# Kernel tuning notes

Measured on AMD Instinct MI355X. Metric: run time of the kernel, lower is better.

## Reference

```python
import jax, jax.numpy as jnp
import numpy as np

I_SIZE = 2048
O_SIZE = 2048
NUM_DOMAINS = 20
B, T = 16, 2048


def setup_inputs() -> dict:
    key = jax.random.key(0)
    k_x, k_w, k_d = jax.random.split(key, 3)
    x = jax.random.normal(k_x, (B, T, I_SIZE), dtype=jnp.float32)
    domain_id = jax.random.randint(k_d, (B,), 0, NUM_DOMAINS)
    # xavier_uniform over [num_domains, O*I]
    limit = float(np.sqrt(6.0 / (NUM_DOMAINS + O_SIZE * I_SIZE)))
    fc_weight = jax.random.uniform(k_w, (NUM_DOMAINS, O_SIZE * I_SIZE), dtype=jnp.float32, minval=-limit, maxval=limit)
    bias_weight = jnp.zeros((NUM_DOMAINS, O_SIZE), dtype=jnp.float32)
    return {"x": x, "domain_id": domain_id, "fc_weight": fc_weight, "bias_weight": bias_weight}


def reference(x, domain_id, fc_weight, bias_weight):
    # Gather per-sample weights: [B, I, O] (flat row reshaped as (I, O))
    W = fc_weight[domain_id].reshape(-1, I_SIZE, O_SIZE)
    b = bias_weight[domain_id]  # [B, O]
    # y = x @ W + b : [B, T, O]
    y = jnp.einsum('bti,bio->bto', x, W) + b[:, None, :]
    return y
```

## Files before the change

### kernel.cpp

```cpp
#include <hip/hip_runtime.h>
#include <hip/hip_bf16.h>
#include <stdint.h>

typedef __attribute__((ext_vector_type(4))) float  f32x4;
typedef __attribute__((ext_vector_type(8))) short  s16x8;
typedef __attribute__((ext_vector_type(4))) short  s16x4;

constexpr int I_SZ = 2048;
constexpr int O_SZ = 2048;
constexpr int T_SZ = 2048;
constexpr int B_MAX = 16;

constexpr size_t XT_ELEMS = (size_t)B_MAX * T_SZ * I_SZ;
constexpr size_t WT_ELEMS = (size_t)B_MAX * I_SZ * O_SZ;
constexpr size_t WS_NEEDED = (XT_ELEMS + WT_ELEMS) * sizeof(short);

__device__ __forceinline__ short f2bf(float f) {
    __hip_bfloat16 h = __float2bfloat16(f);
    return *reinterpret_cast<short*>(&h);
}

__device__ __forceinline__ void gload_lds16(const void* g, void* l) {
    __builtin_amdgcn_global_load_lds(
        (const __attribute__((address_space(1))) unsigned int*)g,
        (__attribute__((address_space(3))) unsigned int*)l, 16, 0, 0);
}

__global__ __launch_bounds__(256) void convA(const float* __restrict__ x,
                                             short* __restrict__ xt) {
    const int c = blockIdx.x * 256 + threadIdx.x;
    const int l  = c & 63;
    const int mi = (c >> 6) & 7;
    const int kt = (c >> 9) & 63;
    const int rest = c >> 15;
    const int mt = rest & 15, bz = rest >> 4;
    const int lr = l & 15, hi = l >> 4;
    const int m = mt * 128 + mi * 16 + lr;
    const float* src = x + ((size_t)(bz * T_SZ + m)) * I_SZ + kt * 32 + 4 * hi;
    f32x4 a = *reinterpret_cast<const f32x4*>(src);
    f32x4 b = *reinterpret_cast<const f32x4*>(src + 16);
    s16x8 h = { f2bf(a[0]), f2bf(a[1]), f2bf(a[2]), f2bf(a[3]),
                f2bf(b[0]), f2bf(b[1]), f2bf(b[2]), f2bf(b[3]) };
    *reinterpret_cast<s16x8*>(xt + (size_t)c * 8) = h;
}

__global__ __launch_bounds__(256) void convB(const float* __restrict__ fcw,
                                             const int* __restrict__ dom_id,
                                             short* __restrict__ wt) {
    const int c = blockIdx.x * 256 + threadIdx.x;
    const int l  = c & 63;
    const int ni = (c >> 6) & 7;
    const int kt = (c >> 9) & 63;
    const int rest = c >> 15;
    const int nt = rest & 15, bz = rest >> 4;
    const int lr = l & 15, hi = l >> 4;
    const int n = nt * 128 + ni * 16 + lr;
    const int dom = dom_id[bz];
    const float* src = fcw + (size_t)dom * ((size_t)I_SZ * O_SZ)
                           + (size_t)(kt * 32 + 4 * hi) * O_SZ + n;
    short h[8];
    #pragma unroll
    for (int j = 0; j < 4; ++j) {
        h[j]     = f2bf(src[(size_t)j * O_SZ]);
        h[4 + j] = f2bf(src[(size_t)(16 + j) * O_SZ]);
    }
    *reinterpret_cast<s16x8*>(wt + (size_t)c * 8) =
        *reinterpret_cast<s16x8*>(h);
}

__global__ __launch_bounds__(256, 2) void gemm_128x256(
        const short* __restrict__ xt, const short* __restrict__ wt,
        const float* __restrict__ bw, const int* __restrict__ dom_id,
        float* __restrict__ out) {
    __shared__ short As[2][8192];

    const int bid = blockIdx.x;
    const int swz = (bid & 7) * 256 + (bid >> 3);
    const int bz = swz >> 7;
    const int mb = (swz >> 3) & 15;
    const int nb = swz & 7;

    const int t = threadIdx.x;
    const int wv = t >> 6, l = t & 63;
    const int lr = l & 15, hi = l >> 4;
    const int nti  = wv >> 1;
    const int bsub = (wv & 1) * 4;

    const short* Abase = xt + (size_t)(bz * 16 + mb) * 64 * 4096;
    const short* Bp = wt + (size_t)((bz * 16 + nb * 2 + nti) * 64) * 4096
                         + bsub * 512 + l * 8;

    auto stageA = [&](int buf, int T) {
        #pragma unroll
        for (int r = 0; r < 4; ++r)
            gload_lds16(Abase + (size_t)(2 * T) * 4096 + r * 2048 + t * 8,
                        &As[buf][r * 2048 + t * 8]);
    };

    f32x4 acc[8][4] = {};

    stageA(0, 0);
    asm volatile("s_waitcnt vmcnt(0)" ::: "memory");
    asm volatile("s_barrier" ::: "memory");

    for (int T = 0; T < 32; ++T) {
        const int d = T & 1;

        s16x8 bq0[4], bq1[4];
        {
            const short* b0 = Bp + (size_t)(2 * T) * 4096;
            #pragma unroll
            for (int g = 0; g < 4; ++g)
                bq0[g] = *reinterpret_cast<const s16x8*>(b0 + g * 512);
            #pragma unroll
            for (int g = 0; g < 4; ++g)
                bq1[g] = *reinterpret_cast<const s16x8*>(b0 + 4096 + g * 512);
        }

        if (T + 1 < 32) stageA(d ^ 1, T + 1);

        s16x8 af[8];
        #pragma unroll
        for (int f = 0; f < 8; ++f)
            af[f] = *reinterpret_cast<const s16x8*>(&As[d][f * 512 + l * 8]);
        __builtin_amdgcn_s_setprio(1);
        #pragma unroll
        for (int f = 0; f < 8; ++f)
            #pragma unroll
            for (int g = 0; g < 4; ++g)
                acc[f][g] = __builtin_amdgcn_mfma_f32_16x16x32_bf16(
                                af[f], bq0[g], acc[f][g], 0, 0, 0);
        __builtin_amdgcn_s_setprio(0);

        #pragma unroll
        for (int f = 0; f < 8; ++f)
            af[f] = *reinterpret_cast<const s16x8*>(&As[d][4096 + f * 512 + l * 8]);
        __builtin_amdgcn_s_setprio(1);
        #pragma unroll
        for (int f = 0; f < 8; ++f)
            #pragma unroll
            for (int g = 0; g < 4; ++g)
                acc[f][g] = __builtin_amdgcn_mfma_f32_16x16x32_bf16(
                                af[f], bq1[g], acc[f][g], 0, 0, 0);
        __builtin_amdgcn_s_setprio(0);

        asm volatile("s_waitcnt vmcnt(0)" ::: "memory");
        asm volatile("s_barrier" ::: "memory");
    }

    const int dom = dom_id[bz];
    const int col0 = nb * 256 + wv * 64;
    float bias[4];
    #pragma unroll
    for (int g = 0; g < 4; ++g)
        bias[g] = bw[dom * O_SZ + col0 + g * 16 + lr];

    const size_t obase = ((size_t)bz * T_SZ + mb * 128) * O_SZ + col0;
    #pragma unroll
    for (int f = 0; f < 8; ++f) {
        #pragma unroll
        for (int r = 0; r < 4; ++r) {
            const int row = f * 16 + hi * 4 + r;
            float* orow = out + obase + (size_t)row * O_SZ;
            #pragma unroll
            for (int g = 0; g < 4; ++g)
                orow[g * 16 + lr] = acc[f][g][r] + bias[g];
        }
    }
}

constexpr int BM = 128, BN = 128, BK = 32;
constexpr int LDK = 40;
constexpr int NKT = I_SZ / BK;

__global__ __launch_bounds__(256) void dal_gemm(
    const float* __restrict__ x, const int* __restrict__ dom_id,
    const float* __restrict__ fcw, const float* __restrict__ bw,
    float* __restrict__ out)
{
    __shared__ short As[2][BM * LDK];
    __shared__ short Bs[2][BN * LDK];
    const int bz = blockIdx.z;
    const int m0 = blockIdx.y * BM, n0 = blockIdx.x * BN;
    const int dom = dom_id[bz];
    const float* Ag = x + ((size_t)bz * T_SZ + m0) * I_SZ;
    const float* Wg = fcw + (size_t)dom * ((size_t)I_SZ * O_SZ) + n0;
    const int t = threadIdx.x;
    const int am = t >> 3, ac = (t & 7) << 2;
    const int bk = (t >> 5) << 2, bn = (t & 31) << 2;
    const int wv = t >> 6, lane = t & 63;
    const int wr = (wv >> 1) << 6, wc = (wv & 1) << 6;
    const int hi = lane >> 4, lr = lane & 15;
    f32x4 acc[4][4] = {};
    f32x4 ra[4], rb[4];
    auto load_tile = [&](int kb) {
        #pragma unroll
        for (int p = 0; p < 4; ++p)
            ra[p] = *reinterpret_cast<const f32x4*>(Ag + (size_t)(am + 32 * p) * I_SZ + kb + ac);
        #pragma unroll
        for (int r = 0; r < 4; ++r)
            rb[r] = *reinterpret_cast<const f32x4*>(Wg + (size_t)(kb + bk + r) * O_SZ + bn);
    };
    auto store_tile = [&](int buf) {
        #pragma unroll
        for (int p = 0; p < 4; ++p) {
            s16x4 h = { f2bf(ra[p][0]), f2bf(ra[p][1]), f2bf(ra[p][2]), f2bf(ra[p][3]) };
            *reinterpret_cast<s16x4*>(&As[buf][(am + 32 * p) * LDK + ac]) = h;
        }
        #pragma unroll
        for (int i = 0; i < 4; ++i) {
            s16x4 h = { f2bf(rb[0][i]), f2bf(rb[1][i]), f2bf(rb[2][i]), f2bf(rb[3][i]) };
            *reinterpret_cast<s16x4*>(&Bs[buf][(bn + i) * LDK + bk]) = h;
        }
    };
    load_tile(0);
    store_tile(0);
    __syncthreads();
    for (int kt = 0; kt < NKT; ++kt) {
        const int cur = kt & 1;
        if (kt + 1 < NKT) load_tile((kt + 1) * BK);
        s16x8 af[4], bfr[4];
        #pragma unroll
        for (int im = 0; im < 4; ++im) {
            const short* p = &As[cur][(wr + im * 16 + lr) * LDK + 4 * hi];
            s16x4 lo = *reinterpret_cast<const s16x4*>(p);
            s16x4 hh = *reinterpret_cast<const s16x4*>(p + 16);
            af[im] = __builtin_shufflevector(lo, hh, 0, 1, 2, 3, 4, 5, 6, 7);
        }
        #pragma unroll
        for (int in = 0; in < 4; ++in) {
            const short* p = &Bs[cur][(wc + in * 16 + lr) * LDK + 4 * hi];
            s16x4 lo = *reinterpret_cast<const s16x4*>(p);
            s16x4 hh = *reinterpret_cast<const s16x4*>(p + 16);
            bfr[in] = __builtin_shufflevector(lo, hh, 0, 1, 2, 3, 4, 5, 6, 7);
        }
        #pragma unroll
        for (int im = 0; im < 4; ++im)
            #pragma unroll
            for (int in = 0; in < 4; ++in)
                acc[im][in] = __builtin_amdgcn_mfma_f32_16x16x32_bf16(
                                  af[im], bfr[in], acc[im][in], 0, 0, 0);
        if (kt + 1 < NKT) store_tile(cur ^ 1);
        __syncthreads();
    }
    float bias[4];
    #pragma unroll
    for (int in = 0; in < 4; ++in)
        bias[in] = bw[dom * O_SZ + n0 + wc + in * 16 + lr];
    const size_t obase = ((size_t)bz * T_SZ + m0) * O_SZ + n0;
    #pragma unroll
    for (int im = 0; im < 4; ++im) {
        #pragma unroll
        for (int r = 0; r < 4; ++r) {
            const int row = wr + im * 16 + hi * 4 + r;
            float* orow = out + obase + (size_t)row * O_SZ;
            #pragma unroll
            for (int in = 0; in < 4; ++in)
                orow[wc + in * 16 + lr] = acc[im][in][r] + bias[in];
        }
    }
}

extern "C" void kernel_launch(void* const* d_in, const int* in_sizes, int n_in,
                              void* d_out, int out_size, void* d_ws, size_t ws_size,
                              hipStream_t stream) {
    const float* x   = (const float*)d_in[0];
    const int*   dom = (const int*)d_in[1];
    const float* fcw = (const float*)d_in[2];
    const float* bw  = (const float*)d_in[3];
    float* out = (float*)d_out;
    const int B = in_sizes[1];

    if (ws_size >= WS_NEEDED && B == B_MAX) {
        short* xt = (short*)d_ws;
        short* wt = xt + XT_ELEMS;
        const int chunks = B * 16 * 64 * 512;
        convA<<<chunks / 256, 256, 0, stream>>>(x, xt);
        convB<<<chunks / 256, 256, 0, stream>>>(fcw, dom, wt);
        gemm_128x256<<<dim3(2048), dim3(256), 0, stream>>>(xt, wt, bw, dom, out);
    } else {
        dim3 grid(O_SZ / BN, T_SZ / BM, B);
        dal_gemm<<<grid, dim3(256), 0, stream>>>(x, dom, fcw, bw, out);
    }
}
```

Baseline: 418.0 us.

## Deepen A staging and software-pipeline B register loads across k-substeps

Doubles the LDS A tile so each stage covers four k-substeps instead of two, halving the number of barriers. B fragments are now double-buffered in registers, and the next substep's loads are issued right after each MFMA group rather than all at the top of the iteration. The top-of-loop wait uses a partial vmcnt so the newest B prefetches can stay in flight past the barrier. In exchange, LDS per block doubles, the final iteration does redundant prefetches, and correctness depends on the manual vmcnt accounting.

```diff
diff --git a/kernel.cpp b/kernel.cpp
--- a/kernel.cpp
+++ b/kernel.cpp
@@ -72,7 +72,7 @@
         const short* __restrict__ xt, const short* __restrict__ wt,
         const float* __restrict__ bw, const int* __restrict__ dom_id,
         float* __restrict__ out) {
-    __shared__ short As[2][8192];
+    __shared__ short As[2][16384];
 
     const int bid = blockIdx.x;
     const int swz = (bid & 7) * 256 + (bid >> 3);
@@ -92,61 +92,70 @@
 
     auto stageA = [&](int buf, int T) {
         #pragma unroll
-        for (int r = 0; r < 4; ++r)
-            gload_lds16(Abase + (size_t)(2 * T) * 4096 + r * 2048 + t * 8,
+        for (int r = 0; r < 8; ++r)
+            gload_lds16(Abase + (size_t)(4 * T) * 4096 + r * 2048 + t * 8,
                         &As[buf][r * 2048 + t * 8]);
     };
 
     f32x4 acc[8][4] = {};
-
-    stageA(0, 0);
-    asm volatile("s_waitcnt vmcnt(0)" ::: "memory");
-    asm volatile("s_barrier" ::: "memory");
-
-    for (int T = 0; T < 32; ++T) {
-        const int d = T & 1;
-
-        s16x8 bq0[4], bq1[4];
-        {
-            const short* b0 = Bp + (size_t)(2 * T) * 4096;
-            #pragma unroll
-            for (int g = 0; g < 4; ++g)
-                bq0[g] = *reinterpret_cast<const s16x8*>(b0 + g * 512);
-            #pragma unroll
-            for (int g = 0; g < 4; ++g)
-                bq1[g] = *reinterpret_cast<const s16x8*>(b0 + 4096 + g * 512);
-        }
-
-        if (T + 1 < 32) stageA(d ^ 1, T + 1);
-
+    s16x8 bqA[4], bqB[4];
+
+    auto loadBA = [&](int T, int ks) {
+        const short* b = Bp + (size_t)(4 * T + ks) * 4096;
+        #pragma unroll
+        for (int g = 0; g < 4; ++g)
+            bqA[g] = *reinterpret_cast<const s16x8*>(b + g * 512);
+    };
+    auto loadBB = [&](int T, int ks) {
+        const short* b = Bp + (size_t)(4 * T + ks) * 4096;
+        #pragma unroll
+        for (int g = 0; g < 4; ++g)
+            bqB[g] = *reinterpret_cast<const s16x8*>(b + g * 512);
+    };
+
+    auto mfma32 = [&](int d, int ks, const s16x8* bq) {
         s16x8 af[8];
         #pragma unroll
         for (int f = 0; f < 8; ++f)
-            af[f] = *reinterpret_cast<const s16x8*>(&As[d][f * 512 + l * 8]);
+            af[f] = *reinterpret_cast<const s16x8*>(
+                        &As[d][ks * 4096 + f * 512 + l * 8]);
         __builtin_amdgcn_s_setprio(1);
         #pragma unroll
         for (int f = 0; f < 8; ++f)
             #pragma unroll
             for (int g = 0; g < 4; ++g)
                 acc[f][g] = __builtin_amdgcn_mfma_f32_16x16x32_bf16(
-                                af[f], bq0[g], acc[f][g], 0, 0, 0);
+                                af[f], bq[g], acc[f][g], 0, 0, 0);
         __builtin_amdgcn_s_setprio(0);
-
-        #pragma unroll
-        for (int f = 0; f < 8; ++f)
-            af[f] = *reinterpret_cast<const s16x8*>(&As[d][4096 + f * 512 + l * 8]);
-        __builtin_amdgcn_s_setprio(1);
-        #pragma unroll
-        for (int f = 0; f < 8; ++f)
-            #pragma unroll
-            for (int g = 0; g < 4; ++g)
-                acc[f][g] = __builtin_amdgcn_mfma_f32_16x16x32_bf16(
-                                af[f], bq1[g], acc[f][g], 0, 0, 0);
-        __builtin_amdgcn_s_setprio(0);
-
-        asm volatile("s_waitcnt vmcnt(0)" ::: "memory");
+    };
+
+    stageA(0, 0);
+    loadBA(0, 0);
+    loadBB(0, 1);
+
+    for (int T = 0; T < 16; ++T) {
+        const int d = T & 1;
+        const int nT = (T + 1 < 16) ? T + 1 : 15;
+
+        asm volatile("s_waitcnt vmcnt(8)" ::: "memory");
         asm volatile("s_barrier" ::: "memory");
-    }
+
+        stageA(d ^ 1, nT);
+
+        mfma32(d, 0, bqA);
+        loadBA(T, 2);
+
+        mfma32(d, 1, bqB);
+        loadBB(T, 3);
+
+        mfma32(d, 2, bqA);
+        loadBA(nT, 0);
+
+        mfma32(d, 3, bqB);
+        loadBB(nT, 1);
+    }
+
+    asm volatile("s_waitcnt vmcnt(0)" ::: "memory");
 
     const int dom = dom_id[bz];
     const int col0 = nb * 256 + wv * 64;
```

Result: faster. 401.6 us (-3.9%).
